# Kernel tuning notes

Measured on AMD Instinct MI355X. Metric: run time of the kernel, lower is better.

## Reference

```python
import jax, jax.numpy as jnp
import numpy as np

V, E, H, B, T = 50257, 300, 512, 4, 512  # vocab, embed(300 fixed), hid_size, batch, max_seq_len


def setup_inputs() -> dict:
    key = jax.random.key(0)
    ks = jax.random.split(key, 12)
    n = lambda k, shp, s: jax.random.normal(k, shp, dtype=jnp.float32) * s
    return {
        "tokens": jax.random.randint(ks[0], (B, T), 0, V),
        "emb_table": n(ks[1], (V, E), 0.02),      # frozen pretrained embedding
        # forward-direction LstmCellWithProjection params (cell_size == hidden_size == H)
        "W_ih_f": n(ks[2], (E, 4 * H), 0.05),     # input_linearity (no bias)
        "W_hh_f": n(ks[3], (H, 4 * H), 0.05),     # state_linearity weight
        "b_f": jnp.zeros((4 * H,), jnp.float32),  # state_linearity bias
        "W_proj_f": n(ks[4], (H, H), 0.05),       # state_projection (no bias)
        # backward direction
        "W_ih_b": n(ks[5], (E, 4 * H), 0.05),
        "W_hh_b": n(ks[6], (H, 4 * H), 0.05),
        "b_b": jnp.zeros((4 * H,), jnp.float32),
        "W_proj_b": n(ks[7], (H, H), 0.05),
        # final vocab projection nn.Linear(H, V)
        "W_lin": n(ks[8], (H, V), 0.02),
        "b_lin": jnp.zeros((V,), jnp.float32),
    }


def _lstm_proj_scan(x, W_ih, W_hh, b, W_proj):
    """ElmoLstm's LstmCellWithProjection over time. x: [B,T,E] -> [B,T,H]."""
    xp = jnp.einsum("bte,eg->btg", x, W_ih)  # precompute input projections [B,T,4H]

    def step(carry, xt):  # xt: [B,4H]
        h, c = carry
        p = xt + h @ W_hh + b
        i = jax.nn.sigmoid(p[:, :H])
        f = jax.nn.sigmoid(p[:, H:2 * H])
        g = jnp.tanh(p[:, 2 * H:3 * H])
        o = jax.nn.sigmoid(p[:, 3 * H:])
        c2 = i * g + f * c
        h2 = (o * jnp.tanh(c2)) @ W_proj  # projected hidden state
        return (h2, c2), h2

    init = (jnp.zeros((x.shape[0], H), x.dtype), jnp.zeros((x.shape[0], H), x.dtype))
    _, hs = jax.lax.scan(step, init, jnp.swapaxes(xp, 0, 1))  # [T,B,H]
    return jnp.swapaxes(hs, 0, 1)  # [B,T,H]


def reference(tokens, emb_table, W_ih_f, W_hh_f, b_f, W_proj_f,
              W_ih_b, W_hh_b, b_b, W_proj_b, W_lin, b_lin):
    x = emb_table[tokens]  # embedding gather [B,T,E]
    fwd = _lstm_proj_scan(x, W_ih_f, W_hh_f, b_f, W_proj_f)
    bwd = _lstm_proj_scan(x[:, ::-1], W_ih_b, W_hh_b, b_b, W_proj_b)[:, ::-1]
    # num_layers == 1 -> enc is (1,B,T,2H); fwd half / bwd half each through shared Linear
    logits_fwd = (fwd @ W_lin + b_lin).reshape(-1, V)  # [B*T, V]
    logits_bwd = (bwd @ W_lin + b_lin).reshape(-1, V)
    return jnp.concatenate([logits_fwd, logits_bwd], axis=0)  # [2*B*T, V]
```

## Files before the change

### kernel.cpp

```cpp
#include <hip/hip_runtime.h>
#include <hip/hip_bf16.h>

typedef unsigned short u16;
typedef unsigned int u32;
typedef unsigned long long u64;
typedef short bf16x8 __attribute__((ext_vector_type(8)));
typedef float f32x4 __attribute__((ext_vector_type(4)));

#define AS1C(p) ((const __attribute__((address_space(1))) void*)(p))
#define AS3(p)  ((__attribute__((address_space(3))) void*)(p))

__device__ __forceinline__ u16 f2bf(float f) {
    union { float f; unsigned u; } v; v.f = f;
    unsigned x = v.u;
    unsigned r = (x + 0x7FFFu + ((x >> 16) & 1u)) >> 16;
    return (u16)r;
}
__device__ __forceinline__ void st_atomic_u32(u32* p, u32 v) {
    __hip_atomic_store(p, v, __ATOMIC_RELAXED, __HIP_MEMORY_SCOPE_AGENT);
}
__device__ __forceinline__ u32 ld_atomic_u32(const u32* p) {
    return __hip_atomic_load(p, __ATOMIC_RELAXED, __HIP_MEMORY_SCOPE_AGENT);
}

__device__ __forceinline__ void tpose_dev(float (*tile)[33],
        const float* __restrict__ in, u16* __restrict__ out,
        int R, int C, int outR, int ldO, int bx, int by) {
    int c0 = bx * 32, r0 = by * 32;
    int tx = threadIdx.x & 31, ty = threadIdx.x >> 5;
#pragma unroll
    for (int yy = 0; yy < 4; ++yy) {
        int r = r0 + ty + yy * 8, cc = c0 + tx;
        tile[ty + yy * 8][tx] = (r < R && cc < C) ? in[(size_t)r * C + cc] : 0.f;
    }
    __syncthreads();
#pragma unroll
    for (int yy = 0; yy < 4; ++yy) {
        int c = c0 + ty + yy * 8, r = r0 + tx;
        if (c < outR && r < ldO) out[(size_t)c * ldO + r] = f2bf(tile[tx][ty + yy * 8]);
    }
    __syncthreads();
}

__global__ __launch_bounds__(256) void prep(
    const int* __restrict__ tokens, const float* __restrict__ emb, u16* __restrict__ xemb,
    const float* __restrict__ W_ih_f, u16* __restrict__ WT_ihf,
    const float* __restrict__ W_ih_b, u16* __restrict__ WT_ihb,
    const float* __restrict__ W_hh_f, u16* __restrict__ WT_hhf,
    const float* __restrict__ W_hh_b, u16* __restrict__ WT_hhb,
    const float* __restrict__ W_proj_f, u16* __restrict__ WprojTf,
    const float* __restrict__ W_proj_b, u16* __restrict__ WprojTb,
    u16* __restrict__ WprojAf, u16* __restrict__ WprojAb,
    const float* __restrict__ W_lin, u16* __restrict__ WT_lin,
    u64* __restrict__ htag, u32* __restrict__ ctr)
{
    __shared__ float tile[32][33];
    int bid = blockIdx.x;
    int tid = threadIdx.x;
    if (bid < 2048) {
        int tok = tokens[bid];
        const float* src = emb + (size_t)tok * 300;
        u16* dst = xemb + (size_t)bid * 320;
        int c = tid;
        if (c < 320) dst[c] = (c < 300) ? f2bf(src[c]) : (u16)0;
        c += 256;
        if (c < 320) dst[c] = (c < 300) ? f2bf(src[c]) : (u16)0;
        return;
    }
    bid -= 2048;
    if (bid < 640)  { tpose_dev(tile, W_ih_f, WT_ihf, 300, 2048, 2048, 320, bid % 64, bid / 64); return; }
    bid -= 640;
    if (bid < 640)  { tpose_dev(tile, W_ih_b, WT_ihb, 300, 2048, 2048, 320, bid % 64, bid / 64); return; }
    bid -= 640;
    if (bid < 1024) { tpose_dev(tile, W_hh_f, WT_hhf, 512, 2048, 2048, 512, bid % 64, bid / 64); return; }
    bid -= 1024;
    if (bid < 1024) { tpose_dev(tile, W_hh_b, WT_hhb, 512, 2048, 2048, 512, bid % 64, bid / 64); return; }
    bid -= 1024;
    if (bid < 256)  { tpose_dev(tile, W_proj_f, WprojTf, 512, 512, 512, 512, bid % 16, bid / 16); return; }
    bid -= 256;
    if (bid < 256)  { tpose_dev(tile, W_proj_b, WprojTb, 512, 512, 512, 512, bid % 16, bid / 16); return; }
    bid -= 256;
    if (bid < 512)  { int i = bid * 512 + tid; WprojAf[i] = f2bf(W_proj_f[i]); WprojAf[i + 256] = f2bf(W_proj_f[i + 256]); return; }
    bid -= 512;
    if (bid < 512)  { int i = bid * 512 + tid; WprojAb[i] = f2bf(W_proj_b[i]); WprojAb[i + 256] = f2bf(W_proj_b[i + 256]); return; }
    bid -= 512;
    if (bid < 25152) { tpose_dev(tile, W_lin, WT_lin, 512, 50257, 50304, 512, bid % 1572, bid / 1572); return; }
    for (int i = tid; i < 2 * 2 * 4 * 256; i += 256) htag[i] = 0ull;
    if (tid < 64) ctr[tid] = 0;
}

struct GemmJob {
    const u16* A; const u16* BT; float* Cf; u16* Cb; const float* bias;
    int M, Nreal, K, ldA, ldB, ldC, arev, orev, orow_base;
};

__device__ __forceinline__ void gemm_body(const GemmJob& j, int m0, int n0,
                                          char* As, char* Bs, int atomicCb) {
    const int tid = threadIdx.x;
    const int lane = tid & 63;
    const int wid = tid >> 6;
    const int wr = wid >> 1, wc = wid & 1;

    f32x4 zero4 = {0.f, 0.f, 0.f, 0.f};
    f32x4 acc[4][4];
#pragma unroll
    for (int i = 0; i < 4; ++i)
#pragma unroll
        for (int jx = 0; jx < 4; ++jx) acc[i][jx] = zero4;

    const int kIters = j.K >> 5;
    const int l15 = lane & 15, kg = lane >> 4;

    const int srow0 = wid * 32 + (lane >> 2);
    const int srow1 = srow0 + 16;
    const int c0 = (lane & 3) ^ (srow0 & 3);
    const int c1 = (lane & 3) ^ (srow1 & 3);
    int ar0 = m0 + srow0, ar1 = m0 + srow1;
    if (j.arev) {
        ar0 = (ar0 & ~511) | (511 - (ar0 & 511));
        ar1 = (ar1 & ~511) | (511 - (ar1 & 511));
    }
    const u16* ga0 = j.A + (size_t)ar0 * j.ldA + c0 * 8;
    const u16* ga1 = j.A + (size_t)ar1 * j.ldA + c1 * 8;
    const u16* gb0 = j.BT + (size_t)(n0 + srow0) * j.ldB + c0 * 8;
    const u16* gb1 = j.BT + (size_t)(n0 + srow1) * j.ldB + c1 * 8;
    char* ldsA0 = As + wid * 2048;
    char* ldsA1 = As + wid * 2048 + 1024;
    char* ldsB0 = Bs + wid * 2048;
    char* ldsB1 = Bs + wid * 2048 + 1024;

    for (int kt = 0; kt < kIters; ++kt) {
        const int k0 = kt * 32;
        __builtin_amdgcn_global_load_lds(AS1C(ga0 + k0), AS3(ldsA0), 16, 0, 0);
        __builtin_amdgcn_global_load_lds(AS1C(ga1 + k0), AS3(ldsA1), 16, 0, 0);
        __builtin_amdgcn_global_load_lds(AS1C(gb0 + k0), AS3(ldsB0), 16, 0, 0);
        __builtin_amdgcn_global_load_lds(AS1C(gb1 + k0), AS3(ldsB1), 16, 0, 0);
        __syncthreads();

        bf16x8 af[4], bfr[4];
#pragma unroll
        for (int mt = 0; mt < 4; ++mt) {
            int r = wr * 64 + mt * 16 + l15;
            af[mt] = *(const bf16x8*)(As + r * 64 + ((kg ^ (r & 3)) * 16));
        }
#pragma unroll
        for (int nt = 0; nt < 4; ++nt) {
            int r = wc * 64 + nt * 16 + l15;
            bfr[nt] = *(const bf16x8*)(Bs + r * 64 + ((kg ^ (r & 3)) * 16));
        }
#pragma unroll
        for (int mt = 0; mt < 4; ++mt)
#pragma unroll
            for (int nt = 0; nt < 4; ++nt)
                acc[mt][nt] = __builtin_amdgcn_mfma_f32_16x16x32_bf16(af[mt], bfr[nt], acc[mt][nt], 0, 0, 0);
        __syncthreads();
    }

#pragma unroll
    for (int nt = 0; nt < 4; ++nt) {
        int col = n0 + wc * 64 + nt * 16 + l15;
        float bv = (j.bias != nullptr && col < j.Nreal) ? j.bias[col] : 0.f;
#pragma unroll
        for (int mt = 0; mt < 4; ++mt) {
#pragma unroll
            for (int jx = 0; jx < 4; ++jx) {
                int m = m0 + wr * 64 + mt * 16 + kg * 4 + jx;
                int om = j.orev ? ((m & ~511) | (511 - (m & 511))) : m;
                om += j.orow_base;
                float v = acc[mt][nt][jx] + bv;
                if (atomicCb) {
                    float pv = __shfl_down(v, 1);
                    if ((l15 & 1) == 0 && col < j.Nreal)
                        st_atomic_u32((u32*)(j.Cb + (size_t)om * j.ldC + col),
                                      (u32)f2bf(v) | ((u32)f2bf(pv) << 16));
                } else if (col < j.Nreal) {
                    if (j.Cf) j.Cf[(size_t)om * j.ldC + col] = v;
                    else      j.Cb[(size_t)om * j.ldC + col] = f2bf(v);
                }
            }
        }
    }
}

__global__ __launch_bounds__(256) void gemm_multi4(GemmJob j0, GemmJob j1, GemmJob j2, GemmJob j3) {
    __shared__ char pool[16384];
    GemmJob j = (blockIdx.z == 0) ? j0 : (blockIdx.z == 1) ? j1 : (blockIdx.z == 2) ? j2 : j3;
    if ((int)blockIdx.y * 128 >= j.M) return;
    gemm_body(j, blockIdx.y * 128, blockIdx.x * 128, pool, pool + 8192, 0);
}

__global__ __launch_bounds__(256) void lstm_fused(
    const float* __restrict__ Wc_f, const float* __restrict__ Wc_b,
    const float* __restrict__ xp_f, const float* __restrict__ xp_b,
    u64* __restrict__ htag,
    u16* __restrict__ hpre_f, u16* __restrict__ hpre_b,
    const u16* __restrict__ WT_lin,
    const u16* __restrict__ WprojTf, const u16* __restrict__ WprojTb,
    u16* __restrict__ hall, const float* __restrict__ b_lin,
    float* __restrict__ out, u32* __restrict__ ctr)
{
    __shared__ char pool[16384];
    const int tid = threadIdx.x;
    int bid = blockIdx.x;

    if (bid >= 64) {
        bid -= 64;
        if (bid < 128) {
            int dir = bid >> 6, r = bid & 63, y = r >> 2, x = r & 3;
            int m0 = y * 128, n0 = x * 128;
            if (tid == 0) {
                while (ld_atomic_u32(&ctr[8 + dir * 4 + (y & 3)]) < 32u) __builtin_amdgcn_s_sleep(32);
            }
            __syncthreads();
            GemmJob j = { dir ? hpre_b : hpre_f, dir ? WprojTb : WprojTf, nullptr, hall, nullptr,
                          2048, 512, 512, 512, 512, 512, 0, dir ? 1 : 0, dir ? 2048 : 0 };
            gemm_body(j, m0, n0, pool, pool + 8192, 1);
            asm volatile("s_waitcnt vmcnt(0)" ::: "memory");
            __syncthreads();
            if (tid == 0) {
                int obrow = j.orow_base + (j.orev ? ((m0 & ~511) | (511 - ((m0 + 127) & 511))) : m0);
                __hip_atomic_fetch_add(&ctr[16 + (obrow >> 7)], 1u, __ATOMIC_RELAXED, __HIP_MEMORY_SCOPE_AGENT);
            }
            return;
        }
        bid -= 128;
        {
            int cid = bid / (393 * 8), rr = bid % (393 * 8), bi = rr / 393, x = rr % 393;
            int band = (bi < 4) ? (bi * 4 + cid) : (16 + (bi - 4) * 4 + (3 - cid));
            if (tid == 0) {
                while (ld_atomic_u32(&ctr[16 + band]) < 4u) __builtin_amdgcn_s_sleep(127);
            }
            __syncthreads();
            GemmJob j = { hall, WT_lin, out, nullptr, b_lin,
                          4096, 50257, 512, 512, 512, 50257, 0, 0, 0 };
            gemm_body(j, band * 128, x * 128, pool, pool + 8192, 0);
            return;
        }
    }

    __builtin_amdgcn_s_setprio(1);
    u16 (*hlds)[4][520] = (u16(*)[4][520])pool;

    const int dir = blockIdx.x >> 5;
    const int blk = blockIdx.x & 31;
    const int lane = tid & 63;
    const int w = tid >> 6;
    const int l15 = lane & 15;
    const int kg = lane >> 4;
    const int gate = l15 & 3;
    const int hloc = w * 4 + (l15 >> 2);

    const float* wcsrc = dir ? Wc_b : Wc_f;
    const float* xp    = dir ? xp_b : xp_f;
    u16* hpre          = dir ? hpre_b : hpre_f;
    u64* ht            = htag + (size_t)dir * 2 * 4 * 256;

    bf16x8 wcf[16];
    {
        const int wccol = gate * 512 + blk * 16 + hloc;
#pragma unroll
        for (int ks = 0; ks < 16; ++ks) {
            bf16x8 wv;
#pragma unroll
            for (int e = 0; e < 8; ++e) {
                int k = ks * 32 + kg * 8 + e;
                wv[e] = (short)f2bf(wcsrc[(size_t)k * 2048 + wccol]);
            }
            wcf[ks] = wv;
        }
    }

    const bf16x8 zero8 = {0, 0, 0, 0, 0, 0, 0, 0};
    float cst[4] = {0.f, 0.f, 0.f, 0.f};

    for (int t = 0; t < 512; ++t) {
        float xpv[4];
        {
            const float* xb = xp + (size_t)t * 2048 + gate * 512 + blk * 16 + hloc;
#pragma unroll
            for (int j = 0; j < 4; ++j) xpv[j] = xb[(size_t)j * 512 * 2048];
        }
        {
            const u64* src = ht + (size_t)(t & 1) * 4 * 256;
            const u64* p0 = src + tid;
            const u64* p1 = src + 256 + tid;
            const u64* p2 = src + 512 + tid;
            const u64* p3 = src + 768 + tid;
            const u32 target = (u32)t;
            u64 w0, w1, w2, w3;
            for (;;) {
                asm volatile(
                    "global_load_dwordx2 %0, %4, off sc0 sc1\n\t"
                    "global_load_dwordx2 %1, %5, off sc0 sc1\n\t"
                    "global_load_dwordx2 %2, %6, off sc0 sc1\n\t"
                    "global_load_dwordx2 %3, %7, off sc0 sc1\n\t"
                    "s_waitcnt vmcnt(0)"
                    : "=&v"(w0), "=&v"(w1), "=&v"(w2), "=&v"(w3)
                    : "v"(p0), "v"(p1), "v"(p2), "v"(p3)
                    : "memory");
                if (((u32)(w0 >> 32) == target) & ((u32)(w1 >> 32) == target) &
                    ((u32)(w2 >> 32) == target) & ((u32)(w3 >> 32) == target)) break;
                __builtin_amdgcn_s_sleep(1);
            }
            asm volatile("" ::: "memory");
            *(u32*)&hlds[t & 1][0][tid * 2] = (u32)w0;
            *(u32*)&hlds[t & 1][1][tid * 2] = (u32)w1;
            *(u32*)&hlds[t & 1][2][tid * 2] = (u32)w2;
            *(u32*)&hlds[t & 1][3][tid * 2] = (u32)w3;
        }
        __syncthreads();

        f32x4 a0 = {0, 0, 0, 0}, a1 = {0, 0, 0, 0};
#pragma unroll
        for (int ks = 0; ks < 16; ++ks) {
            bf16x8 a = zero8;
            if (l15 < 4) a = *(const bf16x8*)&hlds[t & 1][l15][ks * 32 + kg * 8];
            if (ks & 1) a1 = __builtin_amdgcn_mfma_f32_16x16x32_bf16(a, wcf[ks], a1, 0, 0, 0);
            else        a0 = __builtin_amdgcn_mfma_f32_16x16x32_bf16(a, wcf[ks], a0, 0, 0, 0);
        }
        f32x4 accs = a0 + a1;

        float act[4];
#pragma unroll
        for (int j = 0; j < 4; ++j) {
            float x = accs[j] + xpv[j];
            float m = (gate == 2) ? 2.885390082f : -1.442695041f;
            float r = __builtin_amdgcn_rcpf(1.f + __builtin_amdgcn_exp2f(m * x));
            act[j] = (gate == 2) ? (1.f - 2.f * r) : r;
        }
        const int base = lane & ~3;
        float fv[4], gv[4], ov[4];
#pragma unroll
        for (int j = 0; j < 4; ++j) {
            fv[j] = __shfl(act[j], base + 1);
            gv[j] = __shfl(act[j], base + 2);
            ov[j] = __shfl(act[j], base + 3);
        }
        unsigned hbits[4];
#pragma unroll
        for (int j = 0; j < 4; ++j) {
            float c2 = act[j] * gv[j] + fv[j] * cst[j];
            cst[j] = c2;
            float th = 1.f - 2.f * __builtin_amdgcn_rcpf(1.f + __builtin_amdgcn_exp2f(2.885390082f * c2));
            hbits[j] = f2bf(ov[j] * th);
        }
        unsigned pb4[4];
#pragma unroll
        for (int j = 0; j < 4; ++j) pb4[j] = (unsigned)__shfl((int)hbits[j], (lane + 4) & 63);

        if ((lane & 7) == 0 && lane < 16) {
            const int word = blk * 8 + w * 2 + (lane >> 3);
            const int slot = (t + 1) & 1;
#pragma unroll
            for (int j = 0; j < 4; ++j) {
                u32 packed = hbits[j] | (pb4[j] << 16);
                u64 val = ((u64)(u32)(t + 1) << 32) | (u64)packed;
                __hip_atomic_store(&ht[(size_t)(slot * 4 + j) * 256 + word], val,
                                   __ATOMIC_RELAXED, __HIP_MEMORY_SCOPE_AGENT);
                st_atomic_u32((u32*)&hpre[(size_t)(j * 512 + t) * 512 + word * 2], packed);
            }
        }
        if ((t & 127) == 127) {
            asm volatile("s_waitcnt vmcnt(0)" ::: "memory");
            __syncthreads();
            if (tid == 0)
                __hip_atomic_fetch_add(&ctr[8 + dir * 4 + (t >> 7)], 1u,
                                       __ATOMIC_RELAXED, __HIP_MEMORY_SCOPE_AGENT);
        }
    }
}

extern "C" void kernel_launch(void* const* d_in, const int* in_sizes, int n_in,
                              void* d_out, int out_size, void* d_ws, size_t ws_size,
                              hipStream_t stream) {
    const int*   tokens   = (const int*)d_in[0];
    const float* emb      = (const float*)d_in[1];
    const float* W_ih_f   = (const float*)d_in[2];
    const float* W_hh_f   = (const float*)d_in[3];
    const float* b_f      = (const float*)d_in[4];
    const float* W_proj_f = (const float*)d_in[5];
    const float* W_ih_b   = (const float*)d_in[6];
    const float* W_hh_b   = (const float*)d_in[7];
    const float* b_b      = (const float*)d_in[8];
    const float* W_proj_b = (const float*)d_in[9];
    const float* W_lin    = (const float*)d_in[10];
    const float* b_lin    = (const float*)d_in[11];
    float* out = (float*)d_out;

    char* ws = (char*)d_ws;
    size_t off = 0;
    auto alloc = [&](size_t bytes) -> char* {
        char* p = ws + off;
        off = (off + bytes + 255) & ~(size_t)255;
        return p;
    };
    u16* xemb     = (u16*)alloc(2048 * 320 * 2);
    u16* WT_ihf   = (u16*)alloc(2048 * 320 * 2);
    u16* WT_ihb   = (u16*)alloc(2048 * 320 * 2);
    u16* WT_hhf   = (u16*)alloc(2048 * 512 * 2);
    u16* WT_hhb   = (u16*)alloc(2048 * 512 * 2);
    u16* WprojTf  = (u16*)alloc(512 * 512 * 2);
    u16* WprojTb  = (u16*)alloc(512 * 512 * 2);
    u16* WprojAf  = (u16*)alloc(512 * 512 * 2);
    u16* WprojAb  = (u16*)alloc(512 * 512 * 2);
    u16* WT_lin   = (u16*)alloc((size_t)50304 * 512 * 2);
    float* xpf    = (float*)alloc((size_t)2048 * 2048 * 4);
    float* xpb    = (float*)alloc((size_t)2048 * 2048 * 4);
    float* Wc32f  = (float*)alloc((size_t)512 * 2048 * 4);
    float* Wc32b  = (float*)alloc((size_t)512 * 2048 * 4);
    u16* hpref    = (u16*)alloc((size_t)2048 * 512 * 2);
    u16* hpreb    = (u16*)alloc((size_t)2048 * 512 * 2);
    u16* hall     = (u16*)alloc((size_t)4096 * 512 * 2);
    u64* htag     = (u64*)alloc((size_t)2 * 2 * 4 * 256 * 8);
    u32* ctr      = (u32*)alloc(64 * 4);

    prep<<<2048 + 640 + 640 + 1024 + 1024 + 256 + 256 + 512 + 512 + 25152 + 1, 256, 0, stream>>>(
        tokens, emb, xemb,
        W_ih_f, WT_ihf, W_ih_b, WT_ihb,
        W_hh_f, WT_hhf, W_hh_b, WT_hhb,
        W_proj_f, WprojTf, W_proj_b, WprojTb,
        WprojAf, WprojAb, W_lin, WT_lin, htag, ctr);

    GemmJob jxf = {xemb, WT_ihf, xpf, nullptr, b_f, 2048, 2048, 320, 320, 320, 2048, 0, 0, 0};
    GemmJob jxb = {xemb, WT_ihb, xpb, nullptr, b_b, 2048, 2048, 320, 320, 320, 2048, 1, 0, 0};
    GemmJob jwf = {WprojAf, WT_hhf, Wc32f, nullptr, nullptr, 512, 2048, 512, 512, 512, 2048, 0, 0, 0};
    GemmJob jwb = {WprojAb, WT_hhb, Wc32b, nullptr, nullptr, 512, 2048, 512, 512, 512, 2048, 0, 0, 0};
    gemm_multi4<<<dim3(16, 16, 4), 256, 0, stream>>>(jxf, jxb, jwf, jwb);

    lstm_fused<<<64 + 128 + 12576, 256, 0, stream>>>(
        Wc32f, Wc32b, xpf, xpb, htag, hpref, hpreb,
        WT_lin, WprojTf, WprojTb, hall, b_lin, out, ctr);
}
```

Measured before the change: 1.653 ms.

## Place LSTM recurrence blocks on one XCC and poll XCC-local hidden-state tags

Block IDs are remapped so that blockIdx%8 in {0,1} selects the 64 recurrent LSTM blocks, aiming to place both directions on the same XCCs under round-robin dispatch. The other slots in the first 256 blocks carry the projection and vocab GEMM work. Each recurrent block records its XCC ID and checks whether its peers share it. If they do, it polls a second tag buffer with L2-coherent (sc0-only) loads instead of system-coherent sc0 sc1 loads, falling back to the global buffer after 128 tries. The goal is lower per-step cross-block synchronization latency, at the cost of an extra store per step and a reliance on the dispatch mapping, which also raises a memory-visibility risk.

```diff
diff --git a/kernel.cpp b/kernel.cpp
--- a/kernel.cpp
+++ b/kernel.cpp
@@ -52,7 +52,8 @@
     const float* __restrict__ W_proj_b, u16* __restrict__ WprojTb,
     u16* __restrict__ WprojAf, u16* __restrict__ WprojAb,
     const float* __restrict__ W_lin, u16* __restrict__ WT_lin,
-    u64* __restrict__ htag, u32* __restrict__ ctr)
+    u64* __restrict__ htagG, u64* __restrict__ htagL,
+    u32* __restrict__ ctr, u32* __restrict__ xccmap)
 {
     __shared__ float tile[32][33];
     int bid = blockIdx.x;
@@ -85,8 +86,8 @@
     if (bid < 512)  { int i = bid * 512 + tid; WprojAb[i] = f2bf(W_proj_b[i]); WprojAb[i + 256] = f2bf(W_proj_b[i + 256]); return; }
     bid -= 512;
     if (bid < 25152) { tpose_dev(tile, W_lin, WT_lin, 512, 50257, 50304, 512, bid % 1572, bid / 1572); return; }
-    for (int i = tid; i < 2 * 2 * 4 * 256; i += 256) htag[i] = 0ull;
-    if (tid < 64) ctr[tid] = 0;
+    for (int i = tid; i < 2 * 2 * 4 * 256; i += 256) { htagG[i] = 0ull; htagL[i] = 0ull; }
+    if (tid < 64) { ctr[tid] = 0; xccmap[tid] = 0; }
 }
 
 struct GemmJob {
@@ -192,40 +193,46 @@
 __global__ __launch_bounds__(256) void lstm_fused(
     const float* __restrict__ Wc_f, const float* __restrict__ Wc_b,
     const float* __restrict__ xp_f, const float* __restrict__ xp_b,
-    u64* __restrict__ htag,
+    u64* __restrict__ htagG, u64* __restrict__ htagL,
     u16* __restrict__ hpre_f, u16* __restrict__ hpre_b,
     const u16* __restrict__ WT_lin,
     const u16* __restrict__ WprojTf, const u16* __restrict__ WprojTb,
     u16* __restrict__ hall, const float* __restrict__ b_lin,
-    float* __restrict__ out, u32* __restrict__ ctr)
+    float* __restrict__ out, u32* __restrict__ ctr, u32* __restrict__ xccmap)
 {
     __shared__ char pool[16384];
     const int tid = threadIdx.x;
-    int bid = blockIdx.x;
-
-    if (bid >= 64) {
-        bid -= 64;
-        if (bid < 128) {
-            int dir = bid >> 6, r = bid & 63, y = r >> 2, x = r & 3;
-            int m0 = y * 128, n0 = x * 128;
-            if (tid == 0) {
-                while (ld_atomic_u32(&ctr[8 + dir * 4 + (y & 3)]) < 32u) __builtin_amdgcn_s_sleep(32);
-            }
-            __syncthreads();
-            GemmJob j = { dir ? hpre_b : hpre_f, dir ? WprojTb : WprojTf, nullptr, hall, nullptr,
-                          2048, 512, 512, 512, 512, 512, 0, dir ? 1 : 0, dir ? 2048 : 0 };
-            gemm_body(j, m0, n0, pool, pool + 8192, 1);
-            asm volatile("s_waitcnt vmcnt(0)" ::: "memory");
-            __syncthreads();
-            if (tid == 0) {
-                int obrow = j.orow_base + (j.orev ? ((m0 & ~511) | (511 - ((m0 + 127) & 511))) : m0);
-                __hip_atomic_fetch_add(&ctr[16 + (obrow >> 7)], 1u, __ATOMIC_RELAXED, __HIP_MEMORY_SCOPE_AGENT);
-            }
-            return;
-        }
-        bid -= 128;
-        {
-            int cid = bid / (393 * 8), rr = bid % (393 * 8), bi = rr / 393, x = rr % 393;
+    const int bidx = blockIdx.x;
+
+    int dir = 0, blk = 0;
+    {
+        int lid = -1;
+        if (bidx < 256) {
+            int mod8 = bidx & 7, grp = bidx >> 3;
+            if (mod8 >= 6) lid = (mod8 - 6) * 32 + grp;
+            else if (mod8 >= 2) {
+                int pid = (mod8 - 2) * 32 + grp;
+                int pdir = pid >> 6, r = pid & 63, y = r >> 2, x = r & 3;
+                int m0 = y * 128, n0 = x * 128;
+                if (tid == 0) {
+                    while (ld_atomic_u32(&ctr[8 + pdir * 4 + (y & 3)]) < 32u) __builtin_amdgcn_s_sleep(32);
+                }
+                __syncthreads();
+                GemmJob j = { pdir ? hpre_b : hpre_f, pdir ? WprojTb : WprojTf, nullptr, hall, nullptr,
+                              2048, 512, 512, 512, 512, 512, 0, pdir ? 1 : 0, pdir ? 2048 : 0 };
+                gemm_body(j, m0, n0, pool, pool + 8192, 1);
+                asm volatile("s_waitcnt vmcnt(0)" ::: "memory");
+                __syncthreads();
+                if (tid == 0) {
+                    int obrow = j.orow_base + (j.orev ? ((m0 & ~511) | (511 - ((m0 + 127) & 511))) : m0);
+                    __hip_atomic_fetch_add(&ctr[16 + (obrow >> 7)], 1u, __ATOMIC_RELAXED, __HIP_MEMORY_SCOPE_AGENT);
+                }
+                return;
+            } else { dir = mod8; blk = grp; }
+        } else lid = 64 + (bidx - 256);
+
+        if (lid >= 0) {
+            int cid = lid / (393 * 8), rr = lid % (393 * 8), bi = rr / 393, x = rr % 393;
             int band = (bi < 4) ? (bi * 4 + cid) : (16 + (bi - 4) * 4 + (3 - cid));
             if (tid == 0) {
                 while (ld_atomic_u32(&ctr[16 + band]) < 4u) __builtin_amdgcn_s_sleep(127);
@@ -241,8 +248,6 @@
     __builtin_amdgcn_s_setprio(1);
     u16 (*hlds)[4][520] = (u16(*)[4][520])pool;
 
-    const int dir = blockIdx.x >> 5;
-    const int blk = blockIdx.x & 31;
     const int lane = tid & 63;
     const int w = tid >> 6;
     const int l15 = lane & 15;
@@ -253,7 +258,12 @@
     const float* wcsrc = dir ? Wc_b : Wc_f;
     const float* xp    = dir ? xp_b : xp_f;
     u16* hpre          = dir ? hpre_b : hpre_f;
-    u64* ht            = htag + (size_t)dir * 2 * 4 * 256;
+    u64* htg           = htagG + (size_t)dir * 2 * 4 * 256;
+    u64* htl           = htagL + (size_t)dir * 2 * 4 * 256;
+
+    u32 myxcc;
+    asm volatile("s_getreg_b32 %0, hwreg(HW_REG_XCC_ID)" : "=s"(myxcc));
+    if (tid == 0) st_atomic_u32(&xccmap[dir * 32 + blk], myxcc + 1u);
 
     bf16x8 wcf[16];
     {
@@ -268,6 +278,14 @@
             }
             wcf[ks] = wv;
         }
+    }
+
+    bool loc;
+    {
+        u32 pxcc;
+        const u32* pm = &xccmap[dir * 32 + (tid >> 3)];
+        while ((pxcc = ld_atomic_u32(pm)) == 0u) __builtin_amdgcn_s_sleep(1);
+        loc = (pxcc == myxcc + 1u);
     }
 
     const bf16x8 zero8 = {0, 0, 0, 0, 0, 0, 0, 0};
@@ -281,26 +299,51 @@
             for (int j = 0; j < 4; ++j) xpv[j] = xb[(size_t)j * 512 * 2048];
         }
         {
-            const u64* src = ht + (size_t)(t & 1) * 4 * 256;
-            const u64* p0 = src + tid;
-            const u64* p1 = src + 256 + tid;
-            const u64* p2 = src + 512 + tid;
-            const u64* p3 = src + 768 + tid;
             const u32 target = (u32)t;
             u64 w0, w1, w2, w3;
-            for (;;) {
-                asm volatile(
-                    "global_load_dwordx2 %0, %4, off sc0 sc1\n\t"
-                    "global_load_dwordx2 %1, %5, off sc0 sc1\n\t"
-                    "global_load_dwordx2 %2, %6, off sc0 sc1\n\t"
-                    "global_load_dwordx2 %3, %7, off sc0 sc1\n\t"
-                    "s_waitcnt vmcnt(0)"
-                    : "=&v"(w0), "=&v"(w1), "=&v"(w2), "=&v"(w3)
-                    : "v"(p0), "v"(p1), "v"(p2), "v"(p3)
-                    : "memory");
-                if (((u32)(w0 >> 32) == target) & ((u32)(w1 >> 32) == target) &
-                    ((u32)(w2 >> 32) == target) & ((u32)(w3 >> 32) == target)) break;
-                __builtin_amdgcn_s_sleep(1);
+            bool got = false;
+            if (loc) {
+                const u64* s = htl + (size_t)(t & 1) * 4 * 256;
+                const u64* q0 = s + tid;
+                const u64* q1 = s + 256 + tid;
+                const u64* q2 = s + 512 + tid;
+                const u64* q3 = s + 768 + tid;
+                for (int it = 0; it < 128; ++it) {
+                    asm volatile(
+                        "global_load_dwordx2 %0, %4, off sc0\n\t"
+                        "global_load_dwordx2 %1, %5, off sc0\n\t"
+                        "global_load_dwordx2 %2, %6, off sc0\n\t"
+                        "global_load_dwordx2 %3, %7, off sc0\n\t"
+                        "s_waitcnt vmcnt(0)"
+                        : "=&v"(w0), "=&v"(w1), "=&v"(w2), "=&v"(w3)
+                        : "v"(q0), "v"(q1), "v"(q2), "v"(q3)
+                        : "memory");
+                    if (((u32)(w0 >> 32) == target) & ((u32)(w1 >> 32) == target) &
+                        ((u32)(w2 >> 32) == target) & ((u32)(w3 >> 32) == target)) { got = true; break; }
+                    __builtin_amdgcn_s_sleep(1);
+                }
+                if (!got) loc = false;
+            }
+            if (!got) {
+                const u64* s = htg + (size_t)(t & 1) * 4 * 256;
+                const u64* q0 = s + tid;
+                const u64* q1 = s + 256 + tid;
+                const u64* q2 = s + 512 + tid;
+                const u64* q3 = s + 768 + tid;
+                for (;;) {
+                    asm volatile(
+                        "global_load_dwordx2 %0, %4, off sc0 sc1\n\t"
+                        "global_load_dwordx2 %1, %5, off sc0 sc1\n\t"
+                        "global_load_dwordx2 %2, %6, off sc0 sc1\n\t"
+                        "global_load_dwordx2 %3, %7, off sc0 sc1\n\t"
+                        "s_waitcnt vmcnt(0)"
+                        : "=&v"(w0), "=&v"(w1), "=&v"(w2), "=&v"(w3)
+                        : "v"(q0), "v"(q1), "v"(q2), "v"(q3)
+                        : "memory");
+                    if (((u32)(w0 >> 32) == target) & ((u32)(w1 >> 32) == target) &
+                        ((u32)(w2 >> 32) == target) & ((u32)(w3 >> 32) == target)) break;
+                    __builtin_amdgcn_s_sleep(1);
+                }
             }
             asm volatile("" ::: "memory");
             *(u32*)&hlds[t & 1][0][tid * 2] = (u32)w0;
@@ -355,7 +398,9 @@
             for (int j = 0; j < 4; ++j) {
                 u32 packed = hbits[j] | (pb4[j] << 16);
                 u64 val = ((u64)(u32)(t + 1) << 32) | (u64)packed;
-                __hip_atomic_store(&ht[(size_t)(slot * 4 + j) * 256 + word], val,
+                asm volatile("global_store_dwordx2 %0, %1, off"
+                             :: "v"(htl + (size_t)(slot * 4 + j) * 256 + word), "v"(val) : "memory");
+                __hip_atomic_store(&htg[(size_t)(slot * 4 + j) * 256 + word], val,
                                    __ATOMIC_RELAXED, __HIP_MEMORY_SCOPE_AGENT);
                 st_atomic_u32((u32*)&hpre[(size_t)(j * 512 + t) * 512 + word * 2], packed);
             }
@@ -411,15 +456,17 @@
     u16* hpref    = (u16*)alloc((size_t)2048 * 512 * 2);
     u16* hpreb    = (u16*)alloc((size_t)2048 * 512 * 2);
     u16* hall     = (u16*)alloc((size_t)4096 * 512 * 2);
-    u64* htag     = (u64*)alloc((size_t)2 * 2 * 4 * 256 * 8);
+    u64* htagG    = (u64*)alloc((size_t)2 * 2 * 4 * 256 * 8);
+    u64* htagL    = (u64*)alloc((size_t)2 * 2 * 4 * 256 * 8);
     u32* ctr      = (u32*)alloc(64 * 4);
+    u32* xccmap   = (u32*)alloc(64 * 4);
 
     prep<<<2048 + 640 + 640 + 1024 + 1024 + 256 + 256 + 512 + 512 + 25152 + 1, 256, 0, stream>>>(
         tokens, emb, xemb,
         W_ih_f, WT_ihf, W_ih_b, WT_ihb,
         W_hh_f, WT_hhf, W_hh_b, WT_hhb,
         W_proj_f, WprojTf, W_proj_b, WprojTb,
-        WprojAf, WprojAb, W_lin, WT_lin, htag, ctr);
+        WprojAf, WprojAb, W_lin, WT_lin, htagG, htagL, ctr, xccmap);
 
     GemmJob jxf = {xemb, WT_ihf, xpf, nullptr, b_f, 2048, 2048, 320, 320, 320, 2048, 0, 0, 0};
     GemmJob jxb = {xemb, WT_ihb, xpb, nullptr, b_b, 2048, 2048, 320, 320, 320, 2048, 1, 0, 0};
@@ -427,7 +474,7 @@
     GemmJob jwb = {WprojAb, WT_hhb, Wc32b, nullptr, nullptr, 512, 2048, 512, 512, 512, 2048, 0, 0, 0};
     gemm_multi4<<<dim3(16, 16, 4), 256, 0, stream>>>(jxf, jxb, jwf, jwb);
 
-    lstm_fused<<<64 + 128 + 12576, 256, 0, stream>>>(
-        Wc32f, Wc32b, xpf, xpb, htag, hpref, hpreb,
-        WT_lin, WprojTf, WprojTb, hall, b_lin, out, ctr);
-}
+    lstm_fused<<<256 + 12576 - 64, 256, 0, stream>>>(
+        Wc32f, Wc32b, xpf, xpb, htagG, htagL, hpref, hpreb,
+        WT_lin, WprojTf, WprojTb, hall, b_lin, out, ctr, xccmap);
+}
```

After: 2.377 ms. 43.8% more time.
